# Kernel optimization log

Hardware: AMD Instinct MI355X
Metric: run time of the kernel (lower is better)

## Reference

```python
import jax, jax.numpy as jnp
import numpy as np

L, D, H, DK, S, B = 6, 1024, 16, 64, 512, 8
DFF = 4 * D
NEG = -1.0e9


def layer_norm(x, g, b, eps=1e-5):
    mu = jnp.mean(x, axis=-1, keepdims=True)
    var = jnp.var(x, axis=-1, keepdims=True)
    return (x - mu) * jax.lax.rsqrt(var + eps) * g + b


def setup_inputs() -> dict:
    key = jax.random.key(0)
    ks = jax.random.split(key, 16)
    s = 0.02
    inp = {
        "x": jax.random.normal(ks[0], (B, S, D), jnp.float32),
        "mask": jax.random.bernoulli(ks[1], 0.1, (B, S, S)),
        "relation": jax.random.normal(ks[2], (B, S, S), jnp.float32) * 0.1,
        # per-layer params (stacked over L)
        "Wq": jax.random.normal(ks[3], (L, D, H * DK), jnp.float32) * s,
        "Wk": jax.random.normal(ks[4], (L, D, H * DK), jnp.float32) * s,
        "Wv": jax.random.normal(ks[5], (L, D, H * DK), jnp.float32) * s,
        "Wo": jax.random.normal(ks[6], (L, H * DK, D), jnp.float32) * s,
        "bo": jnp.zeros((L, D), jnp.float32),
        "ln_g": jnp.ones((L, D), jnp.float32),   # EncoderLayer.norm (shared pre-attn / pre-FFN)
        "ln_b": jnp.zeros((L, D), jnp.float32),
        "ln2_g": jnp.ones((L, D), jnp.float32),  # AttSubLayerv2.norm
        "ln2_b": jnp.zeros((L, D), jnp.float32),
        "W1": jax.random.normal(ks[7], (L, D, DFF), jnp.float32) * s,
        "b1": jnp.zeros((L, DFF), jnp.float32),
        "W2": jax.random.normal(ks[8], (L, DFF, D), jnp.float32) * s,
        "b2": jnp.zeros((L, D), jnp.float32),
        "lnf_g": jnp.ones((D,), jnp.float32),    # Encoder.norm
        "lnf_b": jnp.zeros((D,), jnp.float32),
    }
    return inp


def reference(x, mask, relation, Wq, Wk, Wv, Wo, bo, ln_g, ln_b, ln2_g, ln2_b,
              W1, b1, W2, b2, lnf_g, lnf_b):
    # dropout layers run in eval mode (identity)
    scale = 1.0 / jnp.sqrt(jnp.asarray(DK, x.dtype))
    h = x
    attns = []
    for l in range(L):
        q_in = layer_norm(h, ln_g[l], ln_b[l])
        # AttSubLayerv2
        def proj(W):
            return jnp.einsum('bsd,de->bse', q_in, W).reshape(h.shape[0], -1, H, DK).transpose(0, 2, 1, 3)
        Q, K, V = proj(Wq[l]), proj(Wk[l]), proj(Wv[l])  # [B,H,S,DK]
        qk = jnp.einsum('bhqd,bhkd->bhqk', Q, K)
        scores = jnp.einsum('bhqk,bkn->bhqn', qk, relation) * scale
        scores = jnp.where(mask[:, None], NEG, scores)
        p = jax.nn.softmax(scores, axis=-1)  # [B,H,S,S]
        att = jnp.einsum('bhqk,bhkd->bhqd', p, V).transpose(0, 2, 1, 3).reshape(h.shape[0], -1, H * DK)
        att = att @ Wo[l] + bo[l]
        att_out = layer_norm(att + q_in, ln2_g[l], ln2_b[l])
        h = h + att_out
        # FFN (pre-norm with shared EncoderLayer norm)
        f = layer_norm(h, ln_g[l], ln_b[l])
        h = h + (jax.nn.relu(f @ W1[l] + b1[l]) @ W2[l] + b2[l])
        attns.append(p)
    out = layer_norm(h, lnf_g, lnf_b)
    return out, jnp.stack(attns)
```

## Files before the change

kernel.cpp:

```cpp
#include <hip/hip_runtime.h>
#include <hip/hip_bf16.h>
#include <stdint.h>

#define LL 6
#define DD 1024
#define HH 16
#define DKK 64
#define SS 512
#define BB 8
#define DFF_ 4096
#define BS (BB*SS)
#define NEGV -1.0e9f

typedef __attribute__((ext_vector_type(8))) short short8;
typedef __attribute__((ext_vector_type(4))) float f32x4;
typedef __attribute__((ext_vector_type(4))) unsigned short ushort4v;

static __device__ __forceinline__ float bf2f(unsigned short u){
  union { unsigned int i; float f; } v; v.i = ((unsigned int)u)<<16; return v.f;
}
static __device__ __forceinline__ unsigned short f2bf(float f){
  union { float f; unsigned int i; } v; v.f=f;
  unsigned int r = v.i + 0x7fff + ((v.i>>16)&1);
  return (unsigned short)(r>>16);
}

static __device__ __forceinline__ void gload16(const void* g, void* l){
  __builtin_amdgcn_global_load_lds((const __attribute__((address_space(1))) unsigned int*)g,
                                   (__attribute__((address_space(3))) unsigned int*)l, 16, 0, 0);
}

struct TrDesc { const float* in; unsigned short* out; long is1,is2,os1,os2; int ldin,ldout,zd,gx,gy; };
struct TrPack { TrDesc d[7]; int cum[8]; };

__global__ void __launch_bounds__(256) tr_multi_k(TrPack P)
{
  __shared__ float t[32][33];
  int bid=blockIdx.x, di=0;
  #pragma unroll
  for(int k=1;k<7;k++) if(bid>=P.cum[k]) di=k;
  TrDesc dd=P.d[di];
  int local=bid-P.cum[di];
  int bx=local%dd.gx; int rest=local/dd.gx;
  int by=rest%dd.gy; int z=rest/dd.gy;
  int z1=z/dd.zd, z2=z%dd.zd;
  const float* ip=dd.in+z1*dd.is1+z2*dd.is2;
  unsigned short* op=dd.out+z1*dd.os1+z2*dd.os2;
  int r0=by*32, c0=bx*32;
  int tx=threadIdx.x, ty=threadIdx.y;
  #pragma unroll
  for(int i=0;i<4;i++)
    t[ty+i*8][tx] = ip[(long)(r0+ty+i*8)*dd.ldin + c0+tx];
  __syncthreads();
  #pragma unroll
  for(int i=0;i<4;i++)
    op[(long)(c0+ty+i*8)*dd.ldout + r0+tx] = f2bf(t[tx][ty+i*8]);
}

__global__ void __launch_bounds__(256) maskpack_k(const int* __restrict__ mask, unsigned* __restrict__ mb)
{
  int idx = blockIdx.x*256 + threadIdx.x;
  int row = idx>>4, w = idx&15;
  const int* mp = mask + (long)row*SS + w*32;
  unsigned v=0;
  #pragma unroll
  for(int i=0;i<32;i++) v |= (mp[i]!=0) ? (1u<<i) : 0u;
  mb[idx]=v;
}

__global__ void __launch_bounds__(256) ln_k(const float* __restrict__ src,
    const float* __restrict__ gw, const float* __restrict__ bw,
    float* __restrict__ outf, unsigned short* __restrict__ outb,
    const float* __restrict__ resid)
{
  long row=blockIdx.x;
  float4 v=((const float4*)(src+row*DD))[threadIdx.x];
  float s=v.x+v.y+v.z+v.w;
  float s2=v.x*v.x+v.y*v.y+v.z*v.z+v.w*v.w;
  #pragma unroll
  for(int o=32;o;o>>=1){ s+=__shfl_xor(s,o); s2+=__shfl_xor(s2,o); }
  __shared__ float red[8];
  int wid=threadIdx.x>>6, lane=threadIdx.x&63;
  if(lane==0){ red[wid]=s; red[4+wid]=s2; }
  __syncthreads();
  s=red[0]+red[1]+red[2]+red[3];
  s2=red[4]+red[5]+red[6]+red[7];
  float mu=s*(1.f/DD);
  float rstd=rsqrtf(s2*(1.f/DD)-mu*mu+1e-5f);
  int c=threadIdx.x*4;
  float4 g4=*(const float4*)(gw+c), b4=*(const float4*)(bw+c);
  float4 o;
  o.x=(v.x-mu)*rstd*g4.x+b4.x;
  o.y=(v.y-mu)*rstd*g4.y+b4.y;
  o.z=(v.z-mu)*rstd*g4.z+b4.z;
  o.w=(v.w-mu)*rstd*g4.w+b4.w;
  if(resid){
    float4 r4=((const float4*)(resid+row*DD))[threadIdx.x];
    o.x+=r4.x; o.y+=r4.y; o.z+=r4.z; o.w+=r4.w;
  }
  if(outf) ((float4*)(outf+row*DD))[threadIdx.x]=o;
  if(outb){
    uint2 pk;
    pk.x=(unsigned)f2bf(o.x)|((unsigned)f2bf(o.y)<<16);
    pk.y=(unsigned)f2bf(o.z)|((unsigned)f2bf(o.w)<<16);
    ((uint2*)(outb+row*DD))[threadIdx.x]=pk;
  }
}

__global__ void __launch_bounds__(256) ln2_k(const float* __restrict__ src,
    const float* __restrict__ resid,
    const float* __restrict__ g2, const float* __restrict__ b2,
    const float* __restrict__ g1, const float* __restrict__ b1,
    float* __restrict__ outf, unsigned short* __restrict__ outb)
{
  long row=blockIdx.x;
  int wid=threadIdx.x>>6, lane=threadIdx.x&63, c=threadIdx.x*4;
  __shared__ float red[8];
  float4 v=((const float4*)(src+row*DD))[threadIdx.x];
  float s=v.x+v.y+v.z+v.w;
  float s2=v.x*v.x+v.y*v.y+v.z*v.z+v.w*v.w;
  #pragma unroll
  for(int o=32;o;o>>=1){ s+=__shfl_xor(s,o); s2+=__shfl_xor(s2,o); }
  if(lane==0){ red[wid]=s; red[4+wid]=s2; }
  __syncthreads();
  s=red[0]+red[1]+red[2]+red[3];
  s2=red[4]+red[5]+red[6]+red[7];
  float mu=s*(1.f/DD);
  float rstd=rsqrtf(s2*(1.f/DD)-mu*mu+1e-5f);
  float4 g4=*(const float4*)(g2+c), b4=*(const float4*)(b2+c);
  float4 r4=((const float4*)(resid+row*DD))[threadIdx.x];
  float4 o;
  o.x=(v.x-mu)*rstd*g4.x+b4.x+r4.x;
  o.y=(v.y-mu)*rstd*g4.y+b4.y+r4.y;
  o.z=(v.z-mu)*rstd*g4.z+b4.z+r4.z;
  o.w=(v.w-mu)*rstd*g4.w+b4.w+r4.w;
  ((float4*)(outf+row*DD))[threadIdx.x]=o;
  s=o.x+o.y+o.z+o.w;
  s2=o.x*o.x+o.y*o.y+o.z*o.z+o.w*o.w;
  #pragma unroll
  for(int of=32;of;of>>=1){ s+=__shfl_xor(s,of); s2+=__shfl_xor(s2,of); }
  __syncthreads();
  if(lane==0){ red[wid]=s; red[4+wid]=s2; }
  __syncthreads();
  s=red[0]+red[1]+red[2]+red[3];
  s2=red[4]+red[5]+red[6]+red[7];
  mu=s*(1.f/DD);
  rstd=rsqrtf(s2*(1.f/DD)-mu*mu+1e-5f);
  g4=*(const float4*)(g1+c); b4=*(const float4*)(b1+c);
  uint2 pk;
  pk.x=(unsigned)f2bf((o.x-mu)*rstd*g4.x+b4.x)|((unsigned)f2bf((o.y-mu)*rstd*g4.y+b4.y)<<16);
  pk.y=(unsigned)f2bf((o.z-mu)*rstd*g4.z+b4.z)|((unsigned)f2bf((o.w-mu)*rstd*g4.w+b4.w)<<16);
  ((uint2*)(outb+row*DD))[threadIdx.x]=pk;
}

struct GemmP {
  const unsigned short* A; long sA1; int ldA;
  const unsigned short* B; long sB1; int ldB;
  float* outF; unsigned short* outB; long sO1; int ldO;
  const float* bias;
  const float* residF; int ldR;
  const unsigned short* residB;
  unsigned short *kt, *vt;
  int K, relu, mb;
};

static __device__ __forceinline__ void xcd_map(int mb,int BM,int BN,int& m0,int& n0){
  const int nwg=gridDim.x, bid=blockIdx.x;
  const int nb=(bid&7)*(nwg>>3)+(bid>>3);
  m0=(nb%mb)*BM; n0=(nb/mb)*BN;
}

__global__ void __launch_bounds__(512,2) gemmA_k(GemmP p)
{
  constexpr int BM=128, BN=128, BK=64;
  constexpr int BUFE=(BM+BN)*BK;
  constexpr int FN=2;
  constexpr int WNT=32;
  __shared__ __align__(16) unsigned short smem[4*BUFE];
  const int tid=threadIdx.x, lane=tid&63, wid=tid>>6;
  const int wr=wid>>2, wc=wid&3;
  const int lr=lane&15, lk=(lane>>4)*8;
  int m0,n0; xcd_map(p.mb,BM,BN,m0,n0);
  const int z=blockIdx.y;
  const unsigned short* Ap=p.A+(long)z*p.sA1;
  const unsigned short* Bp=p.B+(long)z*p.sB1;
  const int NT=p.K/BK;

  const int sr8 = lane>>3;
  const int scol = ((lane&7) ^ sr8) << 3;

  #define STAGEA(T,BI) { \
    const long kb_=(long)(T)*BK; \
    unsigned short* As_=smem+(BI)*BUFE; \
    unsigned short* Bs_=As_+BM*BK; \
    _Pragma("unroll") \
    for(int L=0;L<2;L++){ \
      int r_=L*64+wid*8+sr8; \
      gload16(Ap+(long)(m0+r_)*p.ldA+kb_+scol, As_+L*4096+wid*512); \
    } \
    _Pragma("unroll") \
    for(int L=0;L<2;L++){ \
      int r_=L*64+wid*8+sr8; \
      gload16(Bp+(long)(n0+r_)*p.ldB+kb_+scol, Bs_+L*4096+wid*512); \
    } }

  f32x4 acc[4][FN];
  #pragma unroll
  for(int m=0;m<4;m++)
    #pragma unroll
    for(int n=0;n<FN;n++) acc[m][n]=(f32x4){0.f,0.f,0.f,0.f};

  STAGEA(0,0);
  STAGEA(1,1);
  __syncthreads();

  const int xr = (lr&7)<<3;
  for(int t=0;t<NT;t+=2){
    if(t+2<NT) STAGEA(t+2,(t+2)&3);
    if(t+3<NT) STAGEA(t+3,(t+3)&3);
    #pragma unroll
    for(int u=0;u<2;u++){
      const unsigned short* As=smem+((t+u)&3)*BUFE;
      const unsigned short* Bs=As+BM*BK;
      #pragma unroll
      for(int kk=0;kk<2;kk++){
        short8 a[4], b[FN];
        #pragma unroll
        for(int m=0;m<4;m++)
          a[m]=*(const short8*)(As + (wr*64+m*16+lr)*BK + ((kk*32+lk)^xr));
        #pragma unroll
        for(int n=0;n<FN;n++)
          b[n]=*(const short8*)(Bs + (wc*WNT+n*16+lr)*BK + ((kk*32+lk)^xr));
        __builtin_amdgcn_s_setprio(1);
        #pragma unroll
        for(int m=0;m<4;m++)
          #pragma unroll
          for(int n=0;n<FN;n++)
            acc[m][n]=__builtin_amdgcn_mfma_f32_16x16x32_bf16(a[m],b[n],acc[m][n],0,0,0);
        __builtin_amdgcn_s_setprio(0);
      }
    }
    __syncthreads();
  }
  #undef STAGEA

  const int rl=(lane>>4)*4;
  #pragma unroll
  for(int m=0;m<4;m++){
    int gr0 = m0 + wr*64 + m*16 + rl;
    #pragma unroll
    for(int n=0;n<FN;n++){
      int gc = n0 + wc*WNT + n*16 + lr;
      float bv = p.bias ? p.bias[gc] : 0.f;
      #pragma unroll
      for(int r=0;r<4;r++){
        long ro=(long)(gr0+r);
        float val=acc[m][n][r]+bv;
        if(p.relu) val=fmaxf(val,0.f);
        if(p.residF) val += p.residF[ro*(long)p.ldR+gc];
        if(p.residB) val += bf2f(p.residB[ro*(long)p.ldR+gc]);
        long oo = (long)z*p.sO1 + ro*(long)p.ldO+gc;
        if(p.outF) p.outF[oo]=val;
        if(p.outB) p.outB[oo]=f2bf(val);
      }
    }
  }
}

static inline void launch_gemmA(GemmP& p,int M,int N,int Z,hipStream_t s){
  p.mb=M/128;
  gemmA_k<<<dim3((M/128)*(N/128),Z),dim3(512),0,s>>>(p);
}

template<int MODE>
__global__ void __launch_bounds__(512,1) gemmB_k(GemmP p)
{
  constexpr int BM=256, BN=256, BK=64;
  constexpr int BUFE=(BM+BN)*BK;
  __shared__ __align__(16) unsigned short smem[2*BUFE];
  const int tid=threadIdx.x, lane=tid&63, wid=tid>>6;
  const int wr=wid>>2, wc=wid&3;
  const int lr=lane&15, lk=(lane>>4)*8;
  int m0,n0; xcd_map(p.mb,BM,BN,m0,n0);
  const unsigned short* Ap=p.A;
  const unsigned short* Bp=p.B;
  const int NT=p.K/BK;

  const int sr8 = lane>>3;
  const int scol = ((lane&7) ^ sr8) << 3;

  #define STAGEB(T,BI) { \
    const long kb_=(long)(T)*BK; \
    unsigned short* As_=smem+(BI)*BUFE; \
    unsigned short* Bs_=As_+BM*BK; \
    _Pragma("unroll") \
    for(int L=0;L<4;L++){ \
      int r_=L*64+wid*8+sr8; \
      gload16(Ap+(long)(m0+r_)*p.ldA+kb_+scol, As_+L*4096+wid*512); \
    } \
    _Pragma("unroll") \
    for(int L=0;L<4;L++){ \
      int r_=L*64+wid*8+sr8; \
      gload16(Bp+(long)(n0+r_)*p.ldB+kb_+scol, Bs_+L*4096+wid*512); \
    } }

  f32x4 acc[8][4];
  #pragma unroll
  for(int m=0;m<8;m++)
    #pragma unroll
    for(int n=0;n<4;n++) acc[m][n]=(f32x4){0.f,0.f,0.f,0.f};

  STAGEB(0,0);
  __syncthreads();

  const int xr = (lr&7)<<3;
  for(int t=0;t<NT;t++){
    if(t+1<NT) STAGEB(t+1,(t+1)&1);
    const unsigned short* As=smem+(t&1)*BUFE;
    const unsigned short* Bs=As+BM*BK;
    #pragma unroll
    for(int kk=0;kk<2;kk++){
      short8 a[8], b[4];
      #pragma unroll
      for(int m=0;m<8;m++)
        a[m]=*(const short8*)(As + (wr*128+m*16+lr)*BK + ((kk*32+lk)^xr));
      #pragma unroll
      for(int n=0;n<4;n++)
        b[n]=*(const short8*)(Bs + (wc*64+n*16+lr)*BK + ((kk*32+lk)^xr));
      __builtin_amdgcn_s_setprio(1);
      #pragma unroll
      for(int m=0;m<8;m++)
        #pragma unroll
        for(int n=0;n<4;n++)
          acc[m][n]=__builtin_amdgcn_mfma_f32_16x16x32_bf16(a[m],b[n],acc[m][n],0,0,0);
      __builtin_amdgcn_s_setprio(0);
    }
    __syncthreads();
  }
  #undef STAGEB

  const int rl=(lane>>4)*4;
  if(MODE==1){
    int sec = n0>>10;
    #pragma unroll
    for(int m=0;m<8;m++){
      int gr0 = m0 + wr*128 + m*16 + rl;
      int b = gr0>>9, s0 = gr0&511;
      #pragma unroll
      for(int n=0;n<4;n++){
        int gc = n0 + wc*64 + n*16 + lr;
        if(sec==0){
          #pragma unroll
          for(int r=0;r<4;r++)
            p.outB[(long)(gr0+r)*1024 + gc] = f2bf(acc[m][n][r]);
        } else {
          unsigned short* dst = sec==1 ? p.kt : p.vt;
          int hh=(gc>>6)&15, d=gc&63;
          ushort4v pk;
          pk.x=f2bf(acc[m][n][0]); pk.y=f2bf(acc[m][n][1]);
          pk.z=f2bf(acc[m][n][2]); pk.w=f2bf(acc[m][n][3]);
          *(ushort4v*)(dst + (((long)b*HH+hh)*DKK+d)*SS + s0) = pk;
        }
      }
    }
  } else {
    #pragma unroll
    for(int m=0;m<8;m++){
      int gr0 = m0 + wr*128 + m*16 + rl;
      #pragma unroll
      for(int n=0;n<4;n++){
        int gc = n0 + wc*64 + n*16 + lr;
        float bv = p.bias ? p.bias[gc] : 0.f;
        #pragma unroll
        for(int r=0;r<4;r++){
          long ro=(long)(gr0+r);
          float val=acc[m][n][r]+bv;
          if(p.relu) val=fmaxf(val,0.f);
          if(p.residF) val += p.residF[ro*(long)p.ldR+gc];
          if(p.residB) val += bf2f(p.residB[ro*(long)p.ldR+gc]);
          long oo = ro*(long)p.ldO+gc;
          if(p.outF) p.outF[oo]=val;
          if(p.outB) p.outB[oo]=f2bf(val);
        }
      }
    }
  }
}

template<int MODE>
static inline void launch_gemmB(GemmP& p,int M,int N,hipStream_t s){
  p.mb=M/256;
  gemmB_k<MODE><<<dim3((M/256)*(N/256)),dim3(512),0,s>>>(p);
}

__global__ void __launch_bounds__(512) att_k(const unsigned short* __restrict__ Qb,
    const unsigned short* __restrict__ KRT, float* __restrict__ pout,
    const unsigned* __restrict__ maskb, const unsigned short* __restrict__ Vt,
    unsigned short* __restrict__ attb)
{
  constexpr int BM=128, BK=32, NT=512;
  constexpr int FM=4, FN=8;
  __shared__ __align__(16) char smem[49152];
  unsigned short* As = (unsigned short*)smem;
  unsigned short* Bs = (unsigned short*)(smem+8192);
  unsigned short* Ps = (unsigned short*)smem;
  unsigned short* Vs = (unsigned short*)(smem+32768);
  __shared__ float redmx[BM][4];
  __shared__ float redsm[BM][4];
  int bh = blockIdx.y; int b = bh>>4, h = bh&15;
  const unsigned short* Ap = Qb + (long)b*SS*1024 + h*64;
  const unsigned short* Bp = KRT + (long)b*SS*1024 + h*64;
  int m0 = blockIdx.x*BM;
  int tid=threadIdx.x, lane=tid&63, wid=tid>>6;
  int wr=wid>>2, wc=wid&3;
  f32x4 acc[FM][FN];
  #pragma unroll
  for(int i=0;i<FM;i++)
    #pragma unroll
    for(int j=0;j<FN;j++) acc[i][j]=(f32x4){0.f,0.f,0.f,0.f};
  const int lr=lane&15, lk=(lane>>4)*8;
  for(int k0=0;k0<DKK;k0+=BK){
    { int v=tid;
      gload16(Ap + (long)(m0+(v>>2))*1024 + k0 + (v&3)*8, As + (wid*64)*8); }
    #pragma unroll
    for(int r=0;r<4;r++){
      int v=r*NT+tid;
      gload16(Bp + (long)(v>>2)*1024 + k0 + (v&3)*8, Bs + (r*NT+wid*64)*8);
    }
    __syncthreads();
    short8 af[FM], bfr[FN];
    #pragma unroll
    for(int i=0;i<FM;i++) af[i]=*(const short8*)(As + (wr*64+i*16+lr)*BK + lk);
    #pragma unroll
    for(int j=0;j<FN;j++) bfr[j]=*(const short8*)(Bs + (wc*128+j*16+lr)*BK + lk);
    #pragma unroll
    for(int i=0;i<FM;i++)
      #pragma unroll
      for(int j=0;j<FN;j++)
        acc[i][j]=__builtin_amdgcn_mfma_f32_16x16x32_bf16(af[i],bfr[j],acc[i][j],0,0,0);
    __syncthreads();
  }
  const int rl=(lane>>4)*4;
  #pragma unroll
  for(int i=0;i<FM;i++){
    #pragma unroll
    for(int r=0;r<4;r++){
      int row=wr*64+i*16+rl+r;
      uint4 mw = *((const uint4*)(maskb + ((long)(b*SS+m0+row))*16 + wc*4));
      float m_=-3.4e38f;
      #pragma unroll
      for(int j=0;j<FN;j++){
        unsigned word = (j>>1)==0? mw.x : (j>>1)==1? mw.y : (j>>1)==2? mw.z : mw.w;
        float v = ((word>>(((j&1)<<4)+lr))&1) ? NEGV : acc[i][j][r]*0.125f;
        acc[i][j][r]=v; m_=fmaxf(m_,v);
      }
      #pragma unroll
      for(int o=1;o<16;o<<=1) m_=fmaxf(m_,__shfl_xor(m_,o));
      if(lr==0) redmx[row][wc]=m_;
    }
  }
  __syncthreads();
  #pragma unroll
  for(int i=0;i<FM;i++){
    #pragma unroll
    for(int r=0;r<4;r++){
      int row=wr*64+i*16+rl+r;
      float m_=fmaxf(fmaxf(redmx[row][0],redmx[row][1]),fmaxf(redmx[row][2],redmx[row][3]));
      float s_=0.f;
      #pragma unroll
      for(int j=0;j<FN;j++){
        float e=__expf(acc[i][j][r]-m_);
        acc[i][j][r]=e; s_+=e;
      }
      #pragma unroll
      for(int o=1;o<16;o<<=1) s_+=__shfl_xor(s_,o);
      if(lr==0) redsm[row][wc]=s_;
    }
  }
  __syncthreads();
  #pragma unroll
  for(int i=0;i<FM;i++){
    #pragma unroll
    for(int r=0;r<4;r++){
      int row=wr*64+i*16+rl+r;
      float inv=1.f/(redsm[row][0]+redsm[row][1]+redsm[row][2]+redsm[row][3]);
      long obase=((long)bh*SS + m0+row)*(long)SS;
      #pragma unroll
      for(int j=0;j<FN;j++){
        int col=wc*128+j*16+lr;
        float pv=acc[i][j][r]*inv;
        acc[i][j][r]=pv;
        pout[obase+col]=pv;
      }
    }
  }
  __syncthreads();
  f32x4 attacc[4];
  #pragma unroll
  for(int j=0;j<4;j++) attacc[j]=(f32x4){0.f,0.f,0.f,0.f};
  for(int kc=0;kc<4;kc++){
    #pragma unroll
    for(int r2=0;r2<2;r2++){
      int v=r2*512+tid;
      int d=v>>4, m=v&15;
      int u=m^(d&7);
      gload16(Vt + ((long)bh*64 + d)*512 + kc*128 + u*8, Vs + (r2*512 + wid*64)*8);
    }
    if(wc==kc){
      #pragma unroll
      for(int i=0;i<FM;i++){
        #pragma unroll
        for(int r=0;r<4;r++){
          int row=wr*64+i*16+rl+r;
          #pragma unroll
          for(int j=0;j<FN;j++){
            int col=j*16+lr;
            Ps[row*128 + (col ^ ((row&7)<<3))] = f2bf(acc[i][j][r]);
          }
        }
      }
    }
    __syncthreads();
    #pragma unroll
    for(int kk=0;kk<4;kk++){
      int arow=wid*16+lr;
      short8 paf=*(const short8*)(Ps + arow*128 + ((kk*32+lk) ^ ((arow&7)<<3)));
      #pragma unroll
      for(int j=0;j<4;j++){
        int d=j*16+lr;
        short8 vbf=*(const short8*)(Vs + d*128 + ((kk*32+lk) ^ ((d&7)<<3)));
        attacc[j]=__builtin_amdgcn_mfma_f32_16x16x32_bf16(paf,vbf,attacc[j],0,0,0);
      }
    }
    __syncthreads();
  }
  #pragma unroll
  for(int j=0;j<4;j++){
    #pragma unroll
    for(int r=0;r<4;r++){
      int row = m0 + wid*16 + rl + r;
      attb[((long)b*SS + row)*DD + h*64 + j*16 + lr] = f2bf(attacc[j][r]);
    }
  }
}

extern "C" void kernel_launch(void* const* d_in, const int* in_sizes, int n_in,
                              void* d_out, int out_size, void* d_ws, size_t ws_size,
                              hipStream_t stream)
{
  const float* x    =(const float*)d_in[0];
  const int*   mask =(const int*)d_in[1];
  const float* rel  =(const float*)d_in[2];
  const float* Wq   =(const float*)d_in[3];
  const float* Wk   =(const float*)d_in[4];
  const float* Wv   =(const float*)d_in[5];
  const float* Wo   =(const float*)d_in[6];
  const float* bo   =(const float*)d_in[7];
  const float* ln_g =(const float*)d_in[8];
  const float* ln_b =(const float*)d_in[9];
  const float* ln2_g=(const float*)d_in[10];
  const float* ln2_b=(const float*)d_in[11];
  const float* W1   =(const float*)d_in[12];
  const float* b1   =(const float*)d_in[13];
  const float* W2   =(const float*)d_in[14];
  const float* b2   =(const float*)d_in[15];
  const float* lnf_g=(const float*)d_in[16];
  const float* lnf_b=(const float*)d_in[17];
  float* out=(float*)d_out;

  char* w=(char*)d_ws;
  auto alloc=[&](long bytes)->void*{ void* p=(void*)w; w += (bytes+255)&~255L; return p; };
  unsigned short* WTqkv=(unsigned short*)alloc((long)LL*3072*1024*2);
  unsigned short* WoT  =(unsigned short*)alloc((long)LL*1024*1024*2);
  unsigned short* W1T  =(unsigned short*)alloc((long)LL*DFF_*DD*2);
  unsigned short* W2T  =(unsigned short*)alloc((long)LL*DD*DFF_*2);
  unsigned short* relT =(unsigned short*)alloc((long)BB*SS*SS*2);
  unsigned short* qin_b=(unsigned short*)alloc((long)BS*DD*2);
  unsigned short* Qb   =(unsigned short*)alloc((long)BS*1024*2);
  unsigned short* Vt   =(unsigned short*)alloc((long)BB*HH*DKK*SS*2);
  unsigned short* Kt   =(unsigned short*)alloc((long)BB*HH*DKK*SS*2);
  unsigned short* KRT  =(unsigned short*)alloc((long)BB*SS*1024*2);
  unsigned short* attb =(unsigned short*)alloc((long)BS*DD*2);
  float*          attres=(float*)alloc((long)BS*DD*4);
  unsigned short* gbuf =(unsigned short*)alloc((long)BS*DFF_*2);
  float*          hbuf =(float*)alloc((long)BS*DD*4);
  unsigned*       maskb=(unsigned*)alloc((long)BS*16*4);
  (void)ws_size; (void)in_sizes; (void)n_in; (void)out_size;

  TrPack tp;
  auto set=[&](int i, const float* in, unsigned short* o, int ldin, int ldout,
               long is1, long os1, int zd, long is2, long os2, int gx, int gy){
    tp.d[i]={in,o,is1,is2,os1,os2,ldin,ldout,zd,gx,gy};
  };
  set(0, Wq, WTqkv,           1024,1024,(long)1024*1024,(long)3072*1024,1,0,0, 32,32);
  set(1, Wk, WTqkv+1024*1024, 1024,1024,(long)1024*1024,(long)3072*1024,1,0,0, 32,32);
  set(2, Wv, WTqkv+2048*1024, 1024,1024,(long)1024*1024,(long)3072*1024,1,0,0, 32,32);
  set(3, Wo, WoT,             1024,1024,(long)1024*1024,(long)1024*1024,1,0,0, 32,32);
  set(4, W1, W1T, 4096,1024,(long)1024*4096,(long)1024*4096,1,0,0, 128,32);
  set(5, W2, W2T, 1024,4096,(long)4096*1024,(long)4096*1024,1,0,0, 32,128);
  set(6, rel, relT, 512,512,(long)512*512,(long)512*512,1,0,0, 16,16);
  int nb[7]={32*32*LL,32*32*LL,32*32*LL,32*32*LL,128*32*LL,32*128*LL,16*16*BB};
  tp.cum[0]=0;
  for(int i=0;i<7;i++) tp.cum[i+1]=tp.cum[i]+nb[i];
  tr_multi_k<<<dim3(tp.cum[7]),dim3(32,8),0,stream>>>(tp);
  maskpack_k<<<dim3(BS*16/256),dim3(256),0,stream>>>(mask, maskb);

  const float* hin = x;
  for(int l=0;l<LL;l++){
    ln_k<<<dim3(BS),dim3(256),0,stream>>>(hin, ln_g+l*DD, ln_b+l*DD, (float*)nullptr, qin_b, (const float*)nullptr);
    { GemmP p{}; p.A=qin_b; p.ldA=DD; p.B=WTqkv+(long)l*3072*1024; p.ldB=DD;
      p.outB=Qb; p.kt=Kt; p.vt=Vt; p.K=DD;
      launch_gemmB<1>(p, BS, 3072, stream); }
    { GemmP p{}; p.A=relT; p.sA1=(long)SS*SS; p.ldA=SS;
      p.B=Kt; p.sB1=(long)HH*DKK*SS; p.ldB=SS;
      p.outB=KRT; p.sO1=(long)SS*1024; p.ldO=1024; p.K=SS;
      launch_gemmA(p, SS, 1024, BB, stream); }
    float* attn_l = out + (long)BS*DD + (long)l*BB*HH*SS*SS;
    att_k<<<dim3(SS/128, BB*HH),dim3(512),0,stream>>>(Qb, KRT, attn_l, maskb, Vt, attb);
    { GemmP p{}; p.A=attb; p.ldA=DD; p.B=WoT+(long)l*1024*1024; p.ldB=DD;
      p.outF=attres; p.ldO=DD; p.bias=bo+l*DD;
      p.residB=qin_b; p.ldR=DD; p.K=DD;
      launch_gemmA(p, BS, DD, 1, stream); }
    ln2_k<<<dim3(BS),dim3(256),0,stream>>>(attres, hin, ln2_g+l*DD, ln2_b+l*DD,
        ln_g+l*DD, ln_b+l*DD, hbuf, qin_b);
    { GemmP p{}; p.A=qin_b; p.ldA=DD; p.B=W1T+(long)l*DFF_*DD; p.ldB=DD;
      p.outB=gbuf; p.ldO=DFF_; p.bias=b1+l*DFF_; p.relu=1; p.K=DD;
      launch_gemmB<0>(p, BS, DFF_, stream); }
    { GemmP p{}; p.A=gbuf; p.ldA=DFF_; p.B=W2T+(long)l*DD*DFF_; p.ldB=DFF_;
      p.outF=hbuf; p.ldO=DD; p.bias=b2+l*DD;
      p.residF=hbuf; p.ldR=DD; p.K=DFF_;
      launch_gemmA(p, BS, DD, 1, stream); }
    hin=hbuf;
  }
  ln_k<<<dim3(BS),dim3(256),0,stream>>>(hbuf, lnf_g, lnf_b, out, (unsigned short*)nullptr, (const float*)nullptr);
}
```

Before: 1.981 ms.

## Interleave GEMM global loads with MFMA and store attention-out projection as bf16

In gemmA the second prefetch stage now goes out after the first sub-tile's MFMAs, and in gemmB the B-tile prefetch goes out after the first kk MFMA group, instead of issuing all loads up front. This spreads global-to-LDS traffic across the compute loop to reduce issue bursts and contention. Separately, the Wo projection output (plus residual) is stored as bf16 instead of fp32 and ln2_k reads bf16, halving that intermediate's traffic at some precision cost before the layer norm.

```diff
diff --git a/kernel.cpp b/kernel.cpp
--- a/kernel.cpp
+++ b/kernel.cpp
@@ -107,7 +107,7 @@
   }
 }
 
-__global__ void __launch_bounds__(256) ln2_k(const float* __restrict__ src,
+__global__ void __launch_bounds__(256) ln2_k(const unsigned short* __restrict__ srcb,
     const float* __restrict__ resid,
     const float* __restrict__ g2, const float* __restrict__ b2,
     const float* __restrict__ g1, const float* __restrict__ b1,
@@ -116,7 +116,12 @@
   long row=blockIdx.x;
   int wid=threadIdx.x>>6, lane=threadIdx.x&63, c=threadIdx.x*4;
   __shared__ float red[8];
-  float4 v=((const float4*)(src+row*DD))[threadIdx.x];
+  uint2 pin=((const uint2*)(srcb+row*DD))[threadIdx.x];
+  float4 v;
+  v.x=bf2f((unsigned short)(pin.x&0xffff));
+  v.y=bf2f((unsigned short)(pin.x>>16));
+  v.z=bf2f((unsigned short)(pin.y&0xffff));
+  v.w=bf2f((unsigned short)(pin.y>>16));
   float s=v.x+v.y+v.z+v.w;
   float s2=v.x*v.x+v.y*v.y+v.z*v.z+v.w*v.w;
   #pragma unroll
@@ -217,7 +222,6 @@
   const int xr = (lr&7)<<3;
   for(int t=0;t<NT;t+=2){
     if(t+2<NT) STAGEA(t+2,(t+2)&3);
-    if(t+3<NT) STAGEA(t+3,(t+3)&3);
     #pragma unroll
     for(int u=0;u<2;u++){
       const unsigned short* As=smem+((t+u)&3)*BUFE;
@@ -239,6 +243,7 @@
             acc[m][n]=__builtin_amdgcn_mfma_f32_16x16x32_bf16(a[m],b[n],acc[m][n],0,0,0);
         __builtin_amdgcn_s_setprio(0);
       }
+      if(u==0 && t+3<NT) STAGEA(t+3,(t+3)&3);
     }
     __syncthreads();
   }
@@ -289,15 +294,17 @@
   const int sr8 = lane>>3;
   const int scol = ((lane&7) ^ sr8) << 3;
 
-  #define STAGEB(T,BI) { \
+  #define STAGEB_A(T,BI) { \
     const long kb_=(long)(T)*BK; \
     unsigned short* As_=smem+(BI)*BUFE; \
-    unsigned short* Bs_=As_+BM*BK; \
     _Pragma("unroll") \
     for(int L=0;L<4;L++){ \
       int r_=L*64+wid*8+sr8; \
       gload16(Ap+(long)(m0+r_)*p.ldA+kb_+scol, As_+L*4096+wid*512); \
-    } \
+    } }
+  #define STAGEB_B(T,BI) { \
+    const long kb_=(long)(T)*BK; \
+    unsigned short* Bs_=smem+(BI)*BUFE+BM*BK; \
     _Pragma("unroll") \
     for(int L=0;L<4;L++){ \
       int r_=L*64+wid*8+sr8; \
@@ -310,12 +317,13 @@
     #pragma unroll
     for(int n=0;n<4;n++) acc[m][n]=(f32x4){0.f,0.f,0.f,0.f};
 
-  STAGEB(0,0);
+  STAGEB_A(0,0);
+  STAGEB_B(0,0);
   __syncthreads();
 
   const int xr = (lr&7)<<3;
   for(int t=0;t<NT;t++){
-    if(t+1<NT) STAGEB(t+1,(t+1)&1);
+    if(t+1<NT) STAGEB_A(t+1,(t+1)&1);
     const unsigned short* As=smem+(t&1)*BUFE;
     const unsigned short* Bs=As+BM*BK;
     #pragma unroll
@@ -334,10 +342,12 @@
         for(int n=0;n<4;n++)
           acc[m][n]=__builtin_amdgcn_mfma_f32_16x16x32_bf16(a[m],b[n],acc[m][n],0,0,0);
       __builtin_amdgcn_s_setprio(0);
+      if(kk==0 && t+1<NT) STAGEB_B(t+1,(t+1)&1);
     }
     __syncthreads();
   }
-  #undef STAGEB
+  #undef STAGEB_A
+  #undef STAGEB_B
 
   const int rl=(lane>>4)*4;
   if(MODE==1){
@@ -581,7 +591,7 @@
   unsigned short* Kt   =(unsigned short*)alloc((long)BB*HH*DKK*SS*2);
   unsigned short* KRT  =(unsigned short*)alloc((long)BB*SS*1024*2);
   unsigned short* attb =(unsigned short*)alloc((long)BS*DD*2);
-  float*          attres=(float*)alloc((long)BS*DD*4);
+  unsigned short* attres=(unsigned short*)alloc((long)BS*DD*2);
   unsigned short* gbuf =(unsigned short*)alloc((long)BS*DFF_*2);
   float*          hbuf =(float*)alloc((long)BS*DD*4);
   unsigned*       maskb=(unsigned*)alloc((long)BS*16*4);
@@ -618,7 +628,7 @@
     float* attn_l = out + (long)BS*DD + (long)l*BB*HH*SS*SS;
     att_k<<<dim3(SS/128, BB*HH),dim3(512),0,stream>>>(Qb, KRT, attn_l, maskb, Vt, attb);
     { GemmP p{}; p.A=attb; p.ldA=DD; p.B=WoT+(long)l*1024*1024; p.ldB=DD;
-      p.outF=attres; p.ldO=DD; p.bias=bo+l*DD;
+      p.outB=attres; p.ldO=DD; p.bias=bo+l*DD;
       p.residB=qin_b; p.ldR=DD; p.K=DD;
       launch_gemmA(p, BS, DD, 1, stream); }
     ln2_k<<<dim3(BS),dim3(256),0,stream>>>(attres, hin, ln2_g+l*DD, ln2_b+l*DD,
```

After: 1.956 ms (median of 2 runs). No clear change (-1.2%).
